# Performance work log

Hardware: AMD Instinct MI355X
Metric: run time of the kernel (lower is better)

## Reference

```python
import jax, jax.numpy as jnp
import numpy as np

GRID_MIN, GRID_MAX, GRID_SIZE = -4.0, 4.0, 12
BANDWIDTH = (GRID_MAX - GRID_MIN) / max(GRID_SIZE - 1, 1)  # 8/11


def setup_inputs() -> dict:
    key = jax.random.key(0)
    k1, k2, k3, k4 = jax.random.split(key, 4)
    B, I, O, G = 16384, 512, 512, GRID_SIZE
    x = jax.random.normal(k1, (B, I), dtype=jnp.float32)
    coeff = jax.random.normal(k2, (I, O, G), dtype=jnp.float32) * 0.05
    base_w = jax.random.normal(k3, (O, I), dtype=jnp.float32) * (1.0 / np.sqrt(I))
    base_b = jax.random.normal(k4, (O,), dtype=jnp.float32) * 0.01
    centers = jnp.linspace(GRID_MIN, GRID_MAX, G, dtype=jnp.float32)
    return {"x": x, "coeff": coeff, "base_w": base_w, "base_b": base_b, "centers": centers}


def reference(x, coeff, base_w, base_b, centers):
    # RBF basis: [B, I, G]
    diff = (x[..., None] - centers) / jnp.float32(BANDWIDTH)
    basis = jnp.exp(-0.5 * diff * diff)
    # spline contraction over in_dim and grid: [B, O]
    spline = jnp.einsum('big,iog->bo', basis, coeff)
    # residual base linear (torch Linear: x @ W^T + b)
    return spline + x @ base_w.T + base_b
```

## Files before the change

### kernel.cpp

```cpp
#include <hip/hip_runtime.h>
#include <hip/hip_bf16.h>


#define M_DIM 16384
#define N_DIM 512
#define I_DIM 512
#define KTOT  6656
#define NSTEP 104

typedef short short8 __attribute__((ext_vector_type(8)));
typedef float f32x16 __attribute__((ext_vector_type(16)));
typedef unsigned int u32x4 __attribute__((ext_vector_type(4)));

#define CVTPK(dst, lo, hi) \
  asm("v_cvt_pk_bf16_f32 %0, %1, %2" : "=v"(dst) : "v"(lo), "v"(hi))

__device__ __forceinline__ unsigned short f2bf(float f) {
  union { float f; unsigned int u; } c; c.f = f;
  unsigned int r = (c.u + 0x7FFFu + ((c.u >> 16) & 1)) >> 16;
  return (unsigned short)r;
}

__global__ __launch_bounds__(256) void prep_w(const float* __restrict__ coeff,
                                              const float* __restrict__ base_w,
                                              unsigned short* __restrict__ Wb2) {
  int t = blockIdx.x * 256 + threadIdx.x;
  int e0 = (t & 1) * 4;
  int go = t >> 1;
  int o  = go & 511;
  int g  = go >> 9;
  int k4 = g * 8 + e0;
  int ic = k4 / 832;
  int rem = k4 - ic * 832;
  int slot = rem >> 6;
  int ii = rem & 63;
  int i = ic * 64 + ii;
  float v0, v1, v2, v3;
  if (slot == 0) {
    const float4 bw = *(const float4*)(base_w + (size_t)o * I_DIM + i);
    v0 = bw.x; v1 = bw.y; v2 = bw.z; v3 = bw.w;
  } else {
    int gg = slot - 1;
    const float* cp = coeff + (size_t)i * (N_DIM * 12) + o * 12 + gg;
    v0 = cp[0]; v1 = cp[6144]; v2 = cp[2 * 6144]; v3 = cp[3 * 6144];
  }
  ushort4 s;
  s.x = f2bf(v0); s.y = f2bf(v1); s.z = f2bf(v2); s.w = f2bf(v3);
  *(ushort4*)(Wb2 + (size_t)go * 8 + e0) = s;
}

__global__ __launch_bounds__(512, 2) void kan_gemm(const float* __restrict__ x,
                                                   const unsigned short* __restrict__ Wb2,
                                                   const float* __restrict__ bias,
                                                   float* __restrict__ out) {
  __shared__ unsigned short Asw[2][8 * 128 * 8];
  __shared__ unsigned short Bsw[2][8 * 256 * 8];

  const int tid  = threadIdx.x;
  const int lane = tid & 63;
  const int wid  = tid >> 6;
  const int wm   = wid >> 2, wn = wid & 3;

  const int rb = blockIdx.x >> 1;
  const int cb = blockIdx.x & 1;
  const int M0 = rb * 128;
  const int N0 = cb * 256;

  const int arow = tid & 127;
  const int kgp  = tid >> 7;
  const float* xg = x + (size_t)(M0 + arow) * I_DIM + kgp * 16;
  const int aoff0 = ((kgp * 2) * 128 + arow) * 16;
  const int aoff1 = ((kgp * 2 + 1) * 128 + arow) * 16;

  const unsigned short* bsrc[4];
  int bdst[4];
#pragma unroll
  for (int q = 0; q < 4; ++q) {
    bsrc[q] = Wb2 + ((size_t)wid * 512 + N0 + q * 64 + lane) * 8;
    bdst[q] = (wid * 256 + q * 64) * 16;
  }

  const int l31 = lane & 31;
  const int aBase = ((lane >> 5) * 128 + wm * 64 + l31) * 16;
  const int bBase = ((lane >> 5) * 256 + wn * 64 + l31) * 16;

  f32x16 acc[2][2];
#pragma unroll
  for (int i = 0; i < 2; ++i)
#pragma unroll
    for (int j = 0; j < 2; ++j)
#pragma unroll
      for (int r = 0; r < 16; ++r) acc[i][j][r] = 0.f;

  float4 xq[4];
#pragma unroll
  for (int q = 0; q < 4; ++q) xq[q] = *(const float4*)(xg + q * 4);
  float bb[16], ff[16];
  int gslot = 0, gic = 0;

  auto emitA = [&](char* pA) {
    unsigned int w[8];
    if (gslot == 0) {
      float f[16];
#pragma unroll
      for (int q = 0; q < 4; ++q) {
        f[q*4+0] = xq[q].x; f[q*4+1] = xq[q].y; f[q*4+2] = xq[q].z; f[q*4+3] = xq[q].w;
      }
#pragma unroll
      for (int j = 0; j < 8; ++j) CVTPK(w[j], f[2*j], f[2*j+1]);
      *(u32x4*)(pA + aoff0) = (u32x4){w[0], w[1], w[2], w[3]};
      *(u32x4*)(pA + aoff1) = (u32x4){w[4], w[5], w[6], w[7]};
#pragma unroll
      for (int j = 0; j < 16; ++j) {
        float u = fmaf(f[j], 1.375f, 5.5f);
        bb[j] = exp2f(-0.72134752044448170f * u * u);
        ff[j] = exp2f(fmaf(u, 1.44269504088896340f, -0.72134752044448170f));
      }
      if (gic < 7) {
        const float* xn = xg + (gic + 1) * 64;
#pragma unroll
        for (int q = 0; q < 4; ++q) xq[q] = *(const float4*)(xn + q * 4);
        ++gic;
      }
    } else {
#pragma unroll
      for (int j = 0; j < 8; ++j) CVTPK(w[j], bb[2*j], bb[2*j+1]);
      *(u32x4*)(pA + aoff0) = (u32x4){w[0], w[1], w[2], w[3]};
      *(u32x4*)(pA + aoff1) = (u32x4){w[4], w[5], w[6], w[7]};
#pragma unroll
      for (int j = 0; j < 16; ++j) {
        bb[j] *= ff[j];
        ff[j] *= 0.36787944117144233f;
      }
    }
    gslot = (gslot == 12) ? 0 : gslot + 1;
  };

  emitA((char*)&Asw[0][0]);
#pragma unroll
  for (int q = 0; q < 4; ++q)
    __builtin_amdgcn_global_load_lds(
        (const __attribute__((address_space(1))) void*)(bsrc[q]),
        (__attribute__((address_space(3))) void*)((char*)&Bsw[0][0] + bdst[q]), 16, 0, 0);
  __syncthreads();

  int buf = 0;
  for (int ks = 0; ks < NSTEP; ++ks) {
    const int nxt = buf ^ 1;
    if (ks < NSTEP - 1) {
      const size_t ko = (size_t)(ks + 1) * 32768;
#pragma unroll
      for (int q = 0; q < 4; ++q)
        __builtin_amdgcn_global_load_lds(
            (const __attribute__((address_space(1))) void*)(bsrc[q] + ko),
            (__attribute__((address_space(3))) void*)((char*)&Bsw[nxt][0] + bdst[q]), 16, 0, 0);
      emitA((char*)&Asw[nxt][0]);
    }
    const char* pA = (const char*)&Asw[buf][0];
    const char* pB = (const char*)&Bsw[buf][0];
#pragma unroll
    for (int s = 0; s < 4; ++s) {
      const char* a = pA + aBase + s * 4096;
      const char* b = pB + bBase + s * 8192;
      short8 a0 = *(const short8*)(a);
      short8 a1 = *(const short8*)(a + 512);
      short8 b0 = *(const short8*)(b);
      short8 b1 = *(const short8*)(b + 512);
      acc[0][0] = __builtin_amdgcn_mfma_f32_32x32x16_bf16(a0, b0, acc[0][0], 0, 0, 0);
      acc[0][1] = __builtin_amdgcn_mfma_f32_32x32x16_bf16(a0, b1, acc[0][1], 0, 0, 0);
      acc[1][0] = __builtin_amdgcn_mfma_f32_32x32x16_bf16(a1, b0, acc[1][0], 0, 0, 0);
      acc[1][1] = __builtin_amdgcn_mfma_f32_32x32x16_bf16(a1, b1, acc[1][1], 0, 0, 0);
    }
    __syncthreads();
    buf = nxt;
  }

  float bv[2];
#pragma unroll
  for (int fn = 0; fn < 2; ++fn) bv[fn] = bias[N0 + wn * 64 + fn * 32 + l31];
  const int rbase = (lane >> 5) * 4;
#pragma unroll
  for (int fm = 0; fm < 2; ++fm) {
#pragma unroll
    for (int fn = 0; fn < 2; ++fn) {
      const size_t cix = (size_t)(N0 + wn * 64 + fn * 32 + l31);
#pragma unroll
      for (int r = 0; r < 16; ++r) {
        int row = M0 + wm * 64 + fm * 32 + (r & 3) + 8 * (r >> 2) + rbase;
        out[(size_t)row * N_DIM + cix] = acc[fm][fn][r] + bv[fn];
      }
    }
  }
}

extern "C" void kernel_launch(void* const* d_in, const int* in_sizes, int n_in,
                              void* d_out, int out_size, void* d_ws, size_t ws_size,
                              hipStream_t stream) {
  const float* x      = (const float*)d_in[0];
  const float* coeff  = (const float*)d_in[1];
  const float* base_w = (const float*)d_in[2];
  const float* base_b = (const float*)d_in[3];
  unsigned short* Wb2 = (unsigned short*)d_ws;

  prep_w<<<3328, 256, 0, stream>>>(coeff, base_w, Wb2);
  kan_gemm<<<256, 512, 0, stream>>>(x, Wb2, base_b, (float*)d_out);
}
```

Before: 138.0 us.

## Triple-buffer B with two-stage prefetch and split K-step into half-phases

The B tile buffer grows to a three-slot ring with loads issued two steps ahead. Each K-step is split into two halves that interleave half of the A basis generation and B staging with MFMA groups. Explicit waitcnt, s_barrier, sched_barrier and setprio replace the single __syncthreads per step. The x loads are now issued inline each time a slot-0 step comes up rather than prefetched a step early. The cost is more LDS, more barriers per step, and a possible exposed x-load latency.

New measurement: 171.6 us. 1.24x slower.

```diff
diff --git a/kernel.cpp b/kernel.cpp
--- a/kernel.cpp
+++ b/kernel.cpp
@@ -2,7 +2,6 @@
 #include <hip/hip_bf16.h>
 
 
-#define M_DIM 16384
 #define N_DIM 512
 #define I_DIM 512
 #define KTOT  6656
@@ -54,12 +53,13 @@
                                                    const float* __restrict__ bias,
                                                    float* __restrict__ out) {
   __shared__ unsigned short Asw[2][8 * 128 * 8];
-  __shared__ unsigned short Bsw[2][8 * 256 * 8];
+  __shared__ unsigned short Bsw[3][8 * 256 * 8];
 
   const int tid  = threadIdx.x;
   const int lane = tid & 63;
   const int wid  = tid >> 6;
   const int wm   = wid >> 2, wn = wid & 3;
+  const int l31  = lane & 31, hl = lane >> 5;
 
   const int rb = blockIdx.x >> 1;
   const int cb = blockIdx.x & 1;
@@ -69,8 +69,9 @@
   const int arow = tid & 127;
   const int kgp  = tid >> 7;
   const float* xg = x + (size_t)(M0 + arow) * I_DIM + kgp * 16;
-  const int aoff0 = ((kgp * 2) * 128 + arow) * 16;
-  const int aoff1 = ((kgp * 2 + 1) * 128 + arow) * 16;
+  int aoff[2];
+#pragma unroll
+  for (int h = 0; h < 2; ++h) aoff[h] = ((kgp * 2 + h) * 128 + arow) * 16;
 
   const unsigned short* bsrc[4];
   int bdst[4];
@@ -80,9 +81,18 @@
     bdst[q] = (wid * 256 + q * 64) * 16;
   }
 
-  const int l31 = lane & 31;
-  const int aBase = ((lane >> 5) * 128 + wm * 64 + l31) * 16;
-  const int bBase = ((lane >> 5) * 256 + wn * 64 + l31) * 16;
+#define STAGE2(T_, RING_, H_) do {                                             \
+    const size_t ko_ = (size_t)(T_) * 32768;                                   \
+    char* d_ = (char*)&Bsw[RING_][0];                                          \
+    _Pragma("unroll")                                                          \
+    for (int q_ = 2 * (H_); q_ < 2 * (H_) + 2; ++q_)                           \
+      __builtin_amdgcn_global_load_lds(                                        \
+          (const __attribute__((address_space(1))) void*)(bsrc[q_] + ko_),     \
+          (__attribute__((address_space(3))) void*)(d_ + bdst[q_]), 16, 0, 0); \
+  } while (0)
+
+  const int aBase = (hl * 128 + wm * 64 + l31) * 16;
+  const int bBase = (hl * 256 + wn * 64 + l31) * 16;
 
   f32x16 acc[2][2];
 #pragma unroll
@@ -92,102 +102,126 @@
 #pragma unroll
       for (int r = 0; r < 16; ++r) acc[i][j][r] = 0.f;
 
-  float4 xq[4];
-#pragma unroll
-  for (int q = 0; q < 4; ++q) xq[q] = *(const float4*)(xg + q * 4);
   float bb[16], ff[16];
-  int gslot = 0, gic = 0;
-
-  auto emitA = [&](char* pA) {
-    unsigned int w[8];
-    if (gslot == 0) {
-      float f[16];
-#pragma unroll
-      for (int q = 0; q < 4; ++q) {
-        f[q*4+0] = xq[q].x; f[q*4+1] = xq[q].y; f[q*4+2] = xq[q].z; f[q*4+3] = xq[q].w;
-      }
-#pragma unroll
-      for (int j = 0; j < 8; ++j) CVTPK(w[j], f[2*j], f[2*j+1]);
-      *(u32x4*)(pA + aoff0) = (u32x4){w[0], w[1], w[2], w[3]};
-      *(u32x4*)(pA + aoff1) = (u32x4){w[4], w[5], w[6], w[7]};
-#pragma unroll
-      for (int j = 0; j < 16; ++j) {
-        float u = fmaf(f[j], 1.375f, 5.5f);
-        bb[j] = exp2f(-0.72134752044448170f * u * u);
-        ff[j] = exp2f(fmaf(u, 1.44269504088896340f, -0.72134752044448170f));
-      }
-      if (gic < 7) {
-        const float* xn = xg + (gic + 1) * 64;
-#pragma unroll
-        for (int q = 0; q < 4; ++q) xq[q] = *(const float4*)(xn + q * 4);
-        ++gic;
+
+  auto emit_half = [&](char* pA, bool s0, int eic, int h2) {
+    unsigned int w[4];
+    const int j0 = h2 * 8;
+    if (s0) {
+      const float* xp = xg + (size_t)eic * 64 + h2 * 8;
+      float4 p = *(const float4*)(xp);
+      float4 q = *(const float4*)(xp + 4);
+      float f[8] = {p.x, p.y, p.z, p.w, q.x, q.y, q.z, q.w};
+#pragma unroll
+      for (int j2 = 0; j2 < 4; ++j2) CVTPK(w[j2], f[2 * j2], f[2 * j2 + 1]);
+      *(u32x4*)(pA + aoff[h2]) = (u32x4){w[0], w[1], w[2], w[3]};
+#pragma unroll
+      for (int e = 0; e < 8; ++e) {
+        float u = fmaf(f[e], 1.375f, 5.5f);
+        bb[j0 + e] = exp2f(-0.72134752044448170f * u * u);
+        ff[j0 + e] = exp2f(fmaf(u, 1.44269504088896340f, -0.72134752044448170f));
       }
     } else {
 #pragma unroll
-      for (int j = 0; j < 8; ++j) CVTPK(w[j], bb[2*j], bb[2*j+1]);
-      *(u32x4*)(pA + aoff0) = (u32x4){w[0], w[1], w[2], w[3]};
-      *(u32x4*)(pA + aoff1) = (u32x4){w[4], w[5], w[6], w[7]};
-#pragma unroll
-      for (int j = 0; j < 16; ++j) {
-        bb[j] *= ff[j];
-        ff[j] *= 0.36787944117144233f;
+      for (int j2 = 0; j2 < 4; ++j2) CVTPK(w[j2], bb[j0 + 2 * j2], bb[j0 + 2 * j2 + 1]);
+      *(u32x4*)(pA + aoff[h2]) = (u32x4){w[0], w[1], w[2], w[3]};
+#pragma unroll
+      for (int e = 0; e < 8; ++e) {
+        bb[j0 + e] *= ff[j0 + e];
+        ff[j0 + e] *= 0.36787944117144233f;
       }
     }
-    gslot = (gslot == 12) ? 0 : gslot + 1;
   };
 
-  emitA((char*)&Asw[0][0]);
-#pragma unroll
-  for (int q = 0; q < 4; ++q)
-    __builtin_amdgcn_global_load_lds(
-        (const __attribute__((address_space(1))) void*)(bsrc[q]),
-        (__attribute__((address_space(3))) void*)((char*)&Bsw[0][0] + bdst[q]), 16, 0, 0);
-  __syncthreads();
-
-  int buf = 0;
-  for (int ks = 0; ks < NSTEP; ++ks) {
-    const int nxt = buf ^ 1;
-    if (ks < NSTEP - 1) {
-      const size_t ko = (size_t)(ks + 1) * 32768;
-#pragma unroll
-      for (int q = 0; q < 4; ++q)
-        __builtin_amdgcn_global_load_lds(
-            (const __attribute__((address_space(1))) void*)(bsrc[q] + ko),
-            (__attribute__((address_space(3))) void*)((char*)&Bsw[nxt][0] + bdst[q]), 16, 0, 0);
-      emitA((char*)&Asw[nxt][0]);
-    }
-    const char* pA = (const char*)&Asw[buf][0];
-    const char* pB = (const char*)&Bsw[buf][0];
-#pragma unroll
-    for (int s = 0; s < 4; ++s) {
-      const char* a = pA + aBase + s * 4096;
-      const char* b = pB + bBase + s * 8192;
-      short8 a0 = *(const short8*)(a);
-      short8 a1 = *(const short8*)(a + 512);
-      short8 b0 = *(const short8*)(b);
-      short8 b1 = *(const short8*)(b + 512);
-      acc[0][0] = __builtin_amdgcn_mfma_f32_32x32x16_bf16(a0, b0, acc[0][0], 0, 0, 0);
-      acc[0][1] = __builtin_amdgcn_mfma_f32_32x32x16_bf16(a0, b1, acc[0][1], 0, 0, 0);
-      acc[1][0] = __builtin_amdgcn_mfma_f32_32x32x16_bf16(a1, b0, acc[1][0], 0, 0, 0);
-      acc[1][1] = __builtin_amdgcn_mfma_f32_32x32x16_bf16(a1, b1, acc[1][1], 0, 0, 0);
-    }
-    __syncthreads();
-    buf = nxt;
+#define MFMA_QUAD(AV0, AV1, BV0, BV1)                                              \
+  acc[0][0] = __builtin_amdgcn_mfma_f32_32x32x16_bf16(AV0, BV0, acc[0][0], 0, 0, 0); \
+  acc[0][1] = __builtin_amdgcn_mfma_f32_32x32x16_bf16(AV0, BV1, acc[0][1], 0, 0, 0); \
+  acc[1][0] = __builtin_amdgcn_mfma_f32_32x32x16_bf16(AV1, BV0, acc[1][0], 0, 0, 0); \
+  acc[1][1] = __builtin_amdgcn_mfma_f32_32x32x16_bf16(AV1, BV1, acc[1][1], 0, 0, 0)
+
+  emit_half((char*)&Asw[0][0], true, 0, 0);
+  emit_half((char*)&Asw[0][0], true, 0, 1);
+  STAGE2(0, 0, 0); STAGE2(0, 0, 1);
+  STAGE2(1, 1, 0); STAGE2(1, 1, 1);
+  asm volatile("s_waitcnt vmcnt(4) lgkmcnt(0)" ::: "memory");
+  __builtin_amdgcn_s_barrier();
+
+  int cur3 = 0;
+  int eslot = 1, eic = 0;
+#pragma unroll 1
+  for (int t = 0; t < NSTEP; ++t) {
+    const int abuf = t & 1;
+    const char* pA = (const char*)&Asw[abuf][0];
+    const char* pB = (const char*)&Bsw[cur3][0];
+    char* pAe = (char*)&Asw[abuf ^ 1][0];
+    const bool doEmit  = (t < NSTEP - 1);
+    const bool doStage = (t < NSTEP - 2);
+    const bool s0 = (eslot == 0);
+    int nring = cur3 + 2; if (nring >= 3) nring -= 3;
+
+    {
+      if (doEmit)  emit_half(pAe, s0, eic, 0);
+      if (doStage) STAGE2(t + 2, nring, 0);
+      short8 a00 = *(const short8*)(pA + aBase);
+      short8 a01 = *(const short8*)(pA + aBase + 512);
+      short8 b00 = *(const short8*)(pB + bBase);
+      short8 b01 = *(const short8*)(pB + bBase + 512);
+      short8 a10 = *(const short8*)(pA + aBase + 4096);
+      short8 a11 = *(const short8*)(pA + aBase + 4096 + 512);
+      short8 b10 = *(const short8*)(pB + bBase + 8192);
+      short8 b11 = *(const short8*)(pB + bBase + 8192 + 512);
+      __builtin_amdgcn_s_barrier();
+      asm volatile("s_waitcnt lgkmcnt(0)" ::: "memory");
+      __builtin_amdgcn_sched_barrier(0);
+      __builtin_amdgcn_s_setprio(1);
+      MFMA_QUAD(a00, a01, b00, b01);
+      MFMA_QUAD(a10, a11, b10, b11);
+      __builtin_amdgcn_s_setprio(0);
+      __builtin_amdgcn_sched_barrier(0);
+      __builtin_amdgcn_s_barrier();
+    }
+
+    {
+      if (doEmit)  emit_half(pAe, s0, eic, 1);
+      if (doStage) STAGE2(t + 2, nring, 1);
+      short8 a00 = *(const short8*)(pA + aBase + 2 * 4096);
+      short8 a01 = *(const short8*)(pA + aBase + 2 * 4096 + 512);
+      short8 b00 = *(const short8*)(pB + bBase + 2 * 8192);
+      short8 b01 = *(const short8*)(pB + bBase + 2 * 8192 + 512);
+      short8 a10 = *(const short8*)(pA + aBase + 3 * 4096);
+      short8 a11 = *(const short8*)(pA + aBase + 3 * 4096 + 512);
+      short8 b10 = *(const short8*)(pB + bBase + 3 * 8192);
+      short8 b11 = *(const short8*)(pB + bBase + 3 * 8192 + 512);
+      if (doStage) { asm volatile("s_waitcnt vmcnt(4)" ::: "memory"); }
+      else         { asm volatile("s_waitcnt vmcnt(0)" ::: "memory"); }
+      __builtin_amdgcn_s_barrier();
+      asm volatile("s_waitcnt lgkmcnt(0)" ::: "memory");
+      __builtin_amdgcn_sched_barrier(0);
+      __builtin_amdgcn_s_setprio(1);
+      MFMA_QUAD(a00, a01, b00, b01);
+      MFMA_QUAD(a10, a11, b10, b11);
+      __builtin_amdgcn_s_setprio(0);
+      __builtin_amdgcn_sched_barrier(0);
+      __builtin_amdgcn_s_barrier();
+    }
+
+    if (++eslot == 13) { eslot = 0; ++eic; }
+    cur3 = (cur3 == 2) ? 0 : cur3 + 1;
   }
 
   float bv[2];
 #pragma unroll
-  for (int fn = 0; fn < 2; ++fn) bv[fn] = bias[N0 + wn * 64 + fn * 32 + l31];
-  const int rbase = (lane >> 5) * 4;
-#pragma unroll
-  for (int fm = 0; fm < 2; ++fm) {
-#pragma unroll
-    for (int fn = 0; fn < 2; ++fn) {
-      const size_t cix = (size_t)(N0 + wn * 64 + fn * 32 + l31);
+  for (int fo = 0; fo < 2; ++fo) bv[fo] = bias[N0 + wn * 64 + fo * 32 + l31];
+  const int rbase = 4 * hl;
+#pragma unroll
+  for (int fb = 0; fb < 2; ++fb) {
+#pragma unroll
+    for (int fo = 0; fo < 2; ++fo) {
+      const size_t cix = (size_t)(N0 + wn * 64 + fo * 32 + l31);
 #pragma unroll
       for (int r = 0; r < 16; ++r) {
-        int row = M0 + wm * 64 + fm * 32 + (r & 3) + 8 * (r >> 2) + rbase;
-        out[(size_t)row * N_DIM + cix] = acc[fm][fn][r] + bv[fn];
+        int row = M0 + wm * 64 + fb * 32 + (r & 3) + 8 * (r >> 2) + rbase;
+        out[(size_t)row * N_DIM + cix] = acc[fb][fo][r] + bv[fo];
       }
     }
   }
```
